# Kernel tuning notes

Hardware: AMD Instinct MI355X
Metric: run time of the kernel (lower is better)

Reference implementation:

```python
import jax, jax.numpy as jnp
import numpy as np

DIM = 1024
DIM_HEAD = 64
HEADS = 16
DIM_INNER = DIM_HEAD * HEADS  # 1024


def setup_inputs() -> dict:
    key = jax.random.key(0)
    k1, k2, k3 = jax.random.split(key, 3)
    b, n = 2, 2048
    x = jax.random.normal(k1, (b, n, DIM), dtype=jnp.float32)
    gamma = jnp.ones((DIM,), dtype=jnp.float32)
    # torch Linear weight [out,in] applied as x @ W.T; store pre-transposed [in,out]
    w_qkv = jax.random.normal(k2, (DIM, 3 * DIM_INNER), dtype=jnp.float32) * (DIM ** -0.5)
    w_out = jax.random.normal(k3, (DIM_INNER, DIM), dtype=jnp.float32) * (DIM_INNER ** -0.5)
    return {"x": x, "gamma": gamma, "w_qkv": w_qkv, "w_out": w_out}


def reference(x, gamma, w_qkv, w_out):
    h, d = HEADS, DIM_HEAD
    scale = d ** -0.5
    rms_scale = DIM ** 0.5
    # RMSNorm: F.normalize(x, dim=-1) * sqrt(dim) * gamma  (eps=1e-12 clamp on L2 norm)
    norm = jnp.maximum(jnp.linalg.norm(x, axis=-1, keepdims=True), 1e-12)
    xn = x / norm * rms_scale * gamma
    b, n, _ = x.shape
    qkv = xn @ w_qkv  # [b, n, 3*h*d]
    qkv = qkv.reshape(b, n, 3, h, d)
    q = qkv[:, :, 0].transpose(0, 2, 1, 3) * scale  # [b, h, n, d]
    k = qkv[:, :, 1].transpose(0, 2, 1, 3)
    v = qkv[:, :, 2].transpose(0, 2, 1, 3)
    sim = jnp.einsum('bhid,bhjd->bhij', q, k)  # [b, h, n, n]
    causal_mask = jnp.triu(jnp.ones((n, n), dtype=bool), k=1)
    neg = -jnp.finfo(sim.dtype).max
    sim = jnp.where(causal_mask, neg, sim)
    attn = jax.nn.softmax(sim, axis=-1)
    out = jnp.einsum('bhij,bhjd->bhid', attn, v)  # [b, h, n, d]
    out = out.transpose(0, 2, 1, 3).reshape(b, n, h * d)
    return out @ w_out
```

## Files before the change

kernel.cpp:

```cpp
#include <hip/hip_runtime.h>
#include <hip/hip_bf16.h>

typedef __bf16 bf16x8 __attribute__((ext_vector_type(8)));
typedef short s16x4 __attribute__((ext_vector_type(4)));
typedef float f32x4 __attribute__((ext_vector_type(4)));
typedef unsigned short u16x8 __attribute__((ext_vector_type(8)));

#define MFMA_K32(a, b, c) __builtin_amdgcn_mfma_f32_16x16x32_bf16(a, b, c, 0, 0, 0)

static __device__ __forceinline__ f32x4 mfma_k16(s16x4 a, s16x4 b, f32x4 c) {
#ifdef __HIP_DEVICE_COMPILE__
    return __builtin_amdgcn_mfma_f32_16x16x16bf16_1k(a, b, c, 0, 0, 0);
#else
    return c;
#endif
}

static __device__ __forceinline__ float fast_exp2(float x) {
#ifdef __HIP_DEVICE_COMPILE__
    return __builtin_amdgcn_exp2f(x);
#else
    return x;
#endif
}

static __device__ __forceinline__ void prio_hi() {
#ifdef __HIP_DEVICE_COMPILE__
    __builtin_amdgcn_s_setprio(1);
#endif
}
static __device__ __forceinline__ void prio_lo() {
#ifdef __HIP_DEVICE_COMPILE__
    __builtin_amdgcn_s_setprio(0);
#endif
}

#define GLL16(gp, lp)                                              \
    __builtin_amdgcn_global_load_lds(                              \
        (const __attribute__((address_space(1))) void*)(gp),       \
        (__attribute__((address_space(3))) void*)(lp), 16, 0, 0)

static __device__ __forceinline__ unsigned short f2bf(float f) {
    unsigned int u = __float_as_uint(f);
    u += 0x7fffu + ((u >> 16) & 1u);
    return (unsigned short)(u >> 16);
}

static __device__ __forceinline__ unsigned int cvtpk_bf16(float lo, float hi) {
#if defined(__HIP_DEVICE_COMPILE__) && __has_builtin(__builtin_amdgcn_cvt_pk_bf16_f32)
    typedef __bf16 bf16x2 __attribute__((ext_vector_type(2)));
    bf16x2 r = __builtin_amdgcn_cvt_pk_bf16_f32(lo, hi);
    return __builtin_bit_cast(unsigned int, r);
#else
    return (unsigned int)f2bf(lo) | ((unsigned int)f2bf(hi) << 16);
#endif
}

#define LOG2E 1.44269504088896340736f

__global__ __launch_bounds__(256) void prep_k(
    const float* __restrict__ x, const float* __restrict__ gamma,
    const float* __restrict__ w_qkv, const float* __restrict__ w_out,
    unsigned short* __restrict__ xn, unsigned short* __restrict__ wtq,
    unsigned short* __restrict__ wto) {
    __shared__ float sm[32][33];
    int bid = blockIdx.x, tid = threadIdx.x;
    if (bid < 4096) {
        const float* in;
        unsigned short* out;
        int R = 1024, C, bx, by;
        if (bid < 3072) { in = w_qkv; out = wtq; C = 3072; bx = bid % 96; by = bid / 96; }
        else { int b2 = bid - 3072; in = w_out; out = wto; C = 1024; bx = b2 % 32; by = b2 / 32; }
        int c0 = bx * 32, r0 = by * 32;
        int tr = tid >> 5, tc = tid & 31;
#pragma unroll
        for (int i = 0; i < 4; i++)
            sm[tr + i * 8][tc] = in[(size_t)(r0 + tr + i * 8) * C + c0 + tc];
        __syncthreads();
#pragma unroll
        for (int i = 0; i < 4; i++)
            out[(size_t)(c0 + tr + i * 8) * R + r0 + tc] = f2bf(sm[tc][tr + i * 8]);
    } else {
        int row = bid - 4096;
        const float* xr = x + (size_t)row * 1024;
        float4 v = *(const float4*)(xr + tid * 4);
        float ss = v.x * v.x + v.y * v.y + v.z * v.z + v.w * v.w;
#pragma unroll
        for (int off = 1; off < 64; off <<= 1) ss += __shfl_xor(ss, off, 64);
        if ((tid & 63) == 0) sm[0][tid >> 6] = ss;
        __syncthreads();
        float tot = sm[0][0] + sm[0][1] + sm[0][2] + sm[0][3];
        float f = 32.0f / fmaxf(sqrtf(tot), 1e-12f);
        float4 g = *(const float4*)(gamma + tid * 4);
        uint2 o;
        o.x = cvtpk_bf16(v.x * f * g.x, v.y * f * g.y);
        o.y = cvtpk_bf16(v.z * f * g.z, v.w * f * g.w);
        *(uint2*)(xn + (size_t)row * 1024 + tid * 4) = o;
    }
}

template <int MODE, int BM, int KS>
__global__ __launch_bounds__(256) void gemm_bt_k(
    const unsigned short* __restrict__ A, const unsigned short* __restrict__ BT,
    float* __restrict__ C, unsigned short* __restrict__ qw,
    unsigned short* __restrict__ kw, unsigned short* __restrict__ vw,
    int M, int N, int K) {
    constexpr int RT = 4;
    constexpr int CT = (BM == 128) ? 4 : 2;
    __shared__ unsigned short As[BM][32];
    __shared__ unsigned short Bs[128][32];
    int tid = threadIdx.x;
    int wave = tid >> 6, lane = tid & 63, quad = lane >> 4, l16 = lane & 15;
    int wrb, wcb;
    if constexpr (BM == 128) { wrb = (wave >> 1) * 64; wcb = (wave & 1) * 64; }
    else { wrb = 0; wcb = wave * 32; }
    int m0 = blockIdx.y * BM, n0 = blockIdx.x * 128;
    int k_beg = 0, k_end = K;
    if constexpr (KS > 1) {
        int kz = blockIdx.z;
        k_beg = kz * (K / KS);
        k_end = k_beg + K / KS;
    }
    int lrow = lane >> 2, lcol = (lane & 3) * 8;
    const unsigned short *Ag0, *Ag1 = nullptr;
    if constexpr (BM == 128) {
        Ag0 = A + (size_t)(m0 + wave * 32 + lrow) * K + lcol;
        Ag1 = A + (size_t)(m0 + wave * 32 + 16 + lrow) * K + lcol;
    } else {
        Ag0 = A + (size_t)(m0 + wave * 16 + lrow) * K + lcol;
    }
    const unsigned short* Bg0 = BT + (size_t)(n0 + wave * 32 + lrow) * K + lcol;
    const unsigned short* Bg1 = BT + (size_t)(n0 + wave * 32 + 16 + lrow) * K + lcol;
    f32x4 acc[RT][CT] = {};
    for (int k0 = k_beg; k0 < k_end; k0 += 32) {
        __syncthreads();
        if constexpr (BM == 128) {
            GLL16(Ag0 + k0, &As[wave * 32][0]);
            GLL16(Ag1 + k0, &As[wave * 32 + 16][0]);
        } else {
            GLL16(Ag0 + k0, &As[wave * 16][0]);
        }
        GLL16(Bg0 + k0, &Bs[wave * 32][0]);
        GLL16(Bg1 + k0, &Bs[wave * 32 + 16][0]);
        __syncthreads();
        bf16x8 af[RT], bfr[CT];
#pragma unroll
        for (int t = 0; t < RT; t++)
            af[t] = *(const bf16x8*)&As[wrb + t * 16 + l16][quad * 8];
#pragma unroll
        for (int t = 0; t < CT; t++)
            bfr[t] = *(const bf16x8*)&Bs[wcb + t * 16 + l16][quad * 8];
#pragma unroll
        for (int rt = 0; rt < RT; rt++)
#pragma unroll
            for (int ct = 0; ct < CT; ct++)
                acc[rt][ct] = MFMA_K32(af[rt], bfr[ct], acc[rt][ct]);
    }
#pragma unroll
    for (int rt = 0; rt < RT; rt++) {
        int mb = m0 + wrb + rt * 16 + quad * 4;
        int b = mb >> 11, nn = mb & 2047;
#pragma unroll
        for (int ct = 0; ct < CT; ct++) {
            int col = n0 + wcb + ct * 16 + l16;
            if (MODE == 0) {
                if constexpr (KS > 1) {
#pragma unroll
                    for (int r = 0; r < 4; r++)
                        atomicAdd(&C[(size_t)(mb + r) * N + col], acc[rt][ct][r]);
                } else {
#pragma unroll
                    for (int r = 0; r < 4; r++)
                        C[(size_t)(mb + r) * N + col] = acc[rt][ct][r];
                }
            } else {
                int sec = col >> 10, ci = col & 1023;
                int hh = ci >> 6, dd = ci & 63;
                int bh = b * 16 + hh;
                if (sec == 0) {
#pragma unroll
                    for (int r = 0; r < 4; r++)
                        qw[((size_t)bh * 2048 + nn + r) * 64 + dd] =
                            f2bf(acc[rt][ct][r] * (0.125f * LOG2E));
                } else if (sec == 1) {
#pragma unroll
                    for (int r = 0; r < 4; r++)
                        kw[((size_t)bh * 2048 + nn + r) * 64 + dd] = f2bf(acc[rt][ct][r]);
                } else {
                    uint2 pk;
                    pk.x = cvtpk_bf16(acc[rt][ct][0], acc[rt][ct][1]);
                    pk.y = cvtpk_bf16(acc[rt][ct][2], acc[rt][ct][3]);
                    *(uint2*)&vw[((size_t)bh * 64 + dd) * 2048 + nn] = pk;
                }
            }
        }
    }
}

__global__ __launch_bounds__(512, 4) void attn_k(
    const unsigned short* __restrict__ q, const unsigned short* __restrict__ k,
    const unsigned short* __restrict__ vt, unsigned short* __restrict__ o) {
    __shared__ __align__(16) char smem[38912];
    typedef unsigned short ush;
    ush(*Ks)[2][32][72] = (ush(*)[2][32][72])smem;
    ush(*Vt)[2][64][40] = (ush(*)[2][64][40])(smem + 18432);
    float(*Osm)[68] = (float(*)[68])smem;
    float* msm = (float*)(smem + 18432);
    float* lsm = msm + 64;

    int bh = blockIdx.x;
    int qt = 31 - (int)blockIdx.y;
    int tid = threadIdx.x, wave = tid >> 6, lane = tid & 63;
    int quad = lane >> 4, l16 = lane & 15;
    int g = wave >> 2, wq = wave & 3;
    int b = bh >> 4, h = bh & 15;
    const ush* qg = q + (size_t)bh * 2048 * 64;
    const ush* kg = k + (size_t)bh * 2048 * 64;
    const ush* vg = vt + (size_t)bh * 64 * 2048;

    int ti = wq * 64 + lane;
    int kr = ti >> 3, kc = (ti & 7) * 8;
    int vr = ti >> 2, vc = (ti & 3) * 8;
    const ush* Kg = kg + (size_t)kr * 64 + kc;
    const ush* Vg = vg + (size_t)vr * 2048 + vc;

    int row_l = wq * 16 + l16;
    int q0w = qt * 64 + wq * 16;
    bf16x8 bq[2];
#pragma unroll
    for (int ks = 0; ks < 2; ks++)
        bq[ks] = *(const bf16x8*)&qg[(size_t)(q0w + l16) * 64 + ks * 32 + quad * 8];

    f32x4 ot[4] = {};
    float mrun = -1e30f, lrun = 0.f;
    int nT = qt + 1;
    int kt0 = g ? (qt + 1) : 0;

    u16x8 pk, pv;
    pk = *(const u16x8*)(Kg + (size_t)kt0 * 2048);
    pv = *(const u16x8*)(Vg + kt0 * 32);
    *(u16x8*)&Ks[g][0][kr][kc] = pk;
    *(u16x8*)&Vt[g][0][vr][vc] = pv;
    __syncthreads();

    for (int i = 0; i < nT; i++) {
        int cb = i & 1, kt = kt0 + i;
        bool pf = (i + 1 < nT);
        if (pf) {
            pk = *(const u16x8*)(Kg + (size_t)(kt + 1) * 2048);
            pv = *(const u16x8*)(Vg + (kt + 1) * 32);
        }
        f32x4 sf[2];
        prio_hi();
#pragma unroll
        for (int ct = 0; ct < 2; ct++) {
            bf16x8 ak0 = *(const bf16x8*)&Ks[g][cb][ct * 16 + l16][quad * 8];
            bf16x8 ak1 = *(const bf16x8*)&Ks[g][cb][ct * 16 + l16][32 + quad * 8];
            f32x4 s = {};
            s = MFMA_K32(ak0, bq[0], s);
            s = MFMA_K32(ak1, bq[1], s);
            sf[ct] = s;
        }
        prio_lo();
        if (kt >= 2 * qt) {
#pragma unroll
            for (int ct = 0; ct < 2; ct++)
#pragma unroll
                for (int r = 0; r < 4; r++)
                    if (kt * 32 + ct * 16 + quad * 4 + r > qt * 64 + row_l)
                        sf[ct][r] = -1e30f;
        }
        float t0 = fmaxf(sf[0][0], sf[0][1]), t1 = fmaxf(sf[0][2], sf[0][3]);
        float t2 = fmaxf(sf[1][0], sf[1][1]), t3 = fmaxf(sf[1][2], sf[1][3]);
        float mx_l = fmaxf(fmaxf(t0, t1), fmaxf(t2, t3));
        if (__any(mx_l > mrun + 8.0f)) {
            float mx = fmaxf(mx_l, __shfl_xor(mx_l, 16, 64));
            mx = fmaxf(mx, __shfl_xor(mx, 32, 64));
            float mnew = fmaxf(mrun, mx);
            float al = fast_exp2(mrun - mnew);
            mrun = mnew;
            lrun *= al;
#pragma unroll
            for (int dt = 0; dt < 4; dt++)
#pragma unroll
                for (int r = 0; r < 4; r++) ot[dt][r] *= al;
        }
        float rs = 0.f;
#pragma unroll
        for (int ct = 0; ct < 2; ct++)
#pragma unroll
            for (int r = 0; r < 4; r++) {
                float p = fast_exp2(sf[ct][r] - mrun);
                sf[ct][r] = p;
                rs += p;
            }
        lrun += rs;
        s16x4 bpr[2];
#pragma unroll
        for (int ct = 0; ct < 2; ct++) {
            uint2 u;
            u.x = cvtpk_bf16(sf[ct][0], sf[ct][1]);
            u.y = cvtpk_bf16(sf[ct][2], sf[ct][3]);
            bpr[ct] = __builtin_bit_cast(s16x4, u);
        }
        prio_hi();
#pragma unroll
        for (int dt = 0; dt < 4; dt++) {
#pragma unroll
            for (int ct = 0; ct < 2; ct++) {
                s16x4 av = *(const s16x4*)&Vt[g][cb][dt * 16 + l16][ct * 16 + quad * 4];
                ot[dt] = mfma_k16(av, bpr[ct], ot[dt]);
            }
        }
        prio_lo();
        if (pf) {
            *(u16x8*)&Ks[g][1 - cb][kr][kc] = pk;
            *(u16x8*)&Vt[g][1 - cb][vr][vc] = pv;
        }
        __syncthreads();
    }

    lrun += __shfl_xor(lrun, 16, 64);
    lrun += __shfl_xor(lrun, 32, 64);

    if (g == 1) {
        msm[row_l] = mrun;
        lsm[row_l] = lrun;
#pragma unroll
        for (int dt = 0; dt < 4; dt++)
            *(f32x4*)&Osm[row_l][dt * 16 + quad * 4] = ot[dt];
    }
    __syncthreads();
    if (g == 0) {
        float m1 = msm[row_l], l1 = lsm[row_l];
        float mmax = fmaxf(mrun, m1);
        float a0 = fast_exp2(mrun - mmax), a1 = fast_exp2(m1 - mmax);
        float inv = 1.0f / (a0 * lrun + a1 * l1);
        float s0 = a0 * inv, s1 = a1 * inv;
        size_t rowbase = ((size_t)b * 2048 + qt * 64 + row_l) * 1024 + h * 64;
#pragma unroll
        for (int dt = 0; dt < 4; dt++) {
            f32x4 o1 = *(const f32x4*)&Osm[row_l][dt * 16 + quad * 4];
            uint2 pkk;
            pkk.x = cvtpk_bf16(ot[dt][0] * s0 + o1[0] * s1,
                               ot[dt][1] * s0 + o1[1] * s1);
            pkk.y = cvtpk_bf16(ot[dt][2] * s0 + o1[2] * s1,
                               ot[dt][3] * s0 + o1[3] * s1);
            *(uint2*)&o[rowbase + dt * 16 + quad * 4] = pkk;
        }
    }
}

extern "C" void kernel_launch(void* const* d_in, const int* in_sizes, int n_in,
                              void* d_out, int out_size, void* d_ws, size_t ws_size,
                              hipStream_t stream) {
    const float* x = (const float*)d_in[0];
    const float* gamma = (const float*)d_in[1];
    const float* w_qkv = (const float*)d_in[2];
    const float* w_out = (const float*)d_in[3];
    float* out = (float*)d_out;
    char* ws = (char*)d_ws;

    unsigned short* xn = (unsigned short*)(ws);
    unsigned short* wtq = (unsigned short*)(ws + 8388608);
    unsigned short* wto = (unsigned short*)(ws + 14680064);
    unsigned short* qw = (unsigned short*)(ws + 16777216);
    unsigned short* kw = (unsigned short*)(ws + 25165824);
    unsigned short* vw = (unsigned short*)(ws + 33554432);
    unsigned short* ao = xn;

    hipMemsetAsync(out, 0, (size_t)4096 * 1024 * 4, stream);

    prep_k<<<8192, 256, 0, stream>>>(x, gamma, w_qkv, w_out, xn, wtq, wto);
    gemm_bt_k<1, 128, 1><<<dim3(24, 32), 256, 0, stream>>>(xn, wtq, nullptr, qw, kw, vw,
                                                           4096, 3072, 1024);
    attn_k<<<dim3(32, 32), 512, 0, stream>>>(qw, kw, vw, ao);
    gemm_bt_k<0, 64, 2><<<dim3(8, 64, 2), 256, 0, stream>>>(ao, wto, out, nullptr,
                                                            nullptr, nullptr,
                                                            4096, 1024, 1024);
}
```

Baseline: 204.3 us.

## Use 64-key attention tiles with split-KV halves and drop split-K output GEMM

The attention kernel now processes 64-key tiles instead of 32, so each iteration does twice the MFMA work per barrier. The two wave groups split the key range into halves instead of one group idling past the diagonal, and masking runs only on the diagonal tile. The output projection GEMM no longer uses split-K with atomics, which removes the memset of the output buffer. Shared memory grows to about 72 KB per block, which may cut occupancy, and an idle group still waits at barriers when its half is shorter.

```diff
diff --git a/kernel.cpp b/kernel.cpp
--- a/kernel.cpp
+++ b/kernel.cpp
@@ -200,12 +200,12 @@
 __global__ __launch_bounds__(512, 4) void attn_k(
     const unsigned short* __restrict__ q, const unsigned short* __restrict__ k,
     const unsigned short* __restrict__ vt, unsigned short* __restrict__ o) {
-    __shared__ __align__(16) char smem[38912];
+    __shared__ __align__(16) char smem[73728];
     typedef unsigned short ush;
-    ush(*Ks)[2][32][72] = (ush(*)[2][32][72])smem;
-    ush(*Vt)[2][64][40] = (ush(*)[2][64][40])(smem + 18432);
+    ush(*Ks)[2][64][72] = (ush(*)[2][64][72])smem;
+    ush(*Vt)[2][64][72] = (ush(*)[2][64][72])(smem + 36864);
     float(*Osm)[68] = (float(*)[68])smem;
-    float* msm = (float*)(smem + 18432);
+    float* msm = (float*)(smem + 36864);
     float* lsm = msm + 64;
 
     int bh = blockIdx.x;
@@ -219,10 +219,9 @@
     const ush* vg = vt + (size_t)bh * 64 * 2048;
 
     int ti = wq * 64 + lane;
-    int kr = ti >> 3, kc = (ti & 7) * 8;
-    int vr = ti >> 2, vc = (ti & 3) * 8;
+    int kr = ti >> 2, kc = (ti & 3) * 8;
     const ush* Kg = kg + (size_t)kr * 64 + kc;
-    const ush* Vg = vg + (size_t)vr * 2048 + vc;
+    const ush* Vg = vg + (size_t)kr * 2048 + kc;
 
     int row_l = wq * 16 + l16;
     int q0w = qt * 64 + wq * 16;
@@ -233,89 +232,106 @@
 
     f32x4 ot[4] = {};
     float mrun = -1e30f, lrun = 0.f;
-    int nT = qt + 1;
-    int kt0 = g ? (qt + 1) : 0;
-
-    u16x8 pk, pv;
-    pk = *(const u16x8*)(Kg + (size_t)kt0 * 2048);
-    pv = *(const u16x8*)(Vg + kt0 * 32);
-    *(u16x8*)&Ks[g][0][kr][kc] = pk;
-    *(u16x8*)&Vt[g][0][vr][vc] = pv;
+    int nTot = qt + 1;
+    int nT0 = (nTot + 1) >> 1;
+    int myN = g ? (nTot - nT0) : nT0;
+    int kt0 = g ? nT0 : 0;
+    int L = nT0;
+
+    u16x8 pk0, pk1, pv0, pv1;
+    if (myN > 0) {
+        pk0 = *(const u16x8*)(Kg + (size_t)kt0 * 4096);
+        pk1 = *(const u16x8*)(Kg + (size_t)kt0 * 4096 + 32);
+        pv0 = *(const u16x8*)(Vg + kt0 * 64);
+        pv1 = *(const u16x8*)(Vg + kt0 * 64 + 32);
+        *(u16x8*)&Ks[g][0][kr][kc] = pk0;
+        *(u16x8*)&Ks[g][0][kr][kc + 32] = pk1;
+        *(u16x8*)&Vt[g][0][kr][kc] = pv0;
+        *(u16x8*)&Vt[g][0][kr][kc + 32] = pv1;
+    }
     __syncthreads();
 
-    for (int i = 0; i < nT; i++) {
+    for (int i = 0; i < L; i++) {
         int cb = i & 1, kt = kt0 + i;
-        bool pf = (i + 1 < nT);
+        bool act = (i < myN);
+        bool pf = (i + 1 < myN);
         if (pf) {
-            pk = *(const u16x8*)(Kg + (size_t)(kt + 1) * 2048);
-            pv = *(const u16x8*)(Vg + (kt + 1) * 32);
-        }
-        f32x4 sf[2];
-        prio_hi();
-#pragma unroll
-        for (int ct = 0; ct < 2; ct++) {
-            bf16x8 ak0 = *(const bf16x8*)&Ks[g][cb][ct * 16 + l16][quad * 8];
-            bf16x8 ak1 = *(const bf16x8*)&Ks[g][cb][ct * 16 + l16][32 + quad * 8];
-            f32x4 s = {};
-            s = MFMA_K32(ak0, bq[0], s);
-            s = MFMA_K32(ak1, bq[1], s);
-            sf[ct] = s;
-        }
-        prio_lo();
-        if (kt >= 2 * qt) {
-#pragma unroll
-            for (int ct = 0; ct < 2; ct++)
-#pragma unroll
-                for (int r = 0; r < 4; r++)
-                    if (kt * 32 + ct * 16 + quad * 4 + r > qt * 64 + row_l)
-                        sf[ct][r] = -1e30f;
-        }
-        float t0 = fmaxf(sf[0][0], sf[0][1]), t1 = fmaxf(sf[0][2], sf[0][3]);
-        float t2 = fmaxf(sf[1][0], sf[1][1]), t3 = fmaxf(sf[1][2], sf[1][3]);
-        float mx_l = fmaxf(fmaxf(t0, t1), fmaxf(t2, t3));
-        if (__any(mx_l > mrun + 8.0f)) {
-            float mx = fmaxf(mx_l, __shfl_xor(mx_l, 16, 64));
-            mx = fmaxf(mx, __shfl_xor(mx, 32, 64));
-            float mnew = fmaxf(mrun, mx);
-            float al = fast_exp2(mrun - mnew);
-            mrun = mnew;
-            lrun *= al;
-#pragma unroll
-            for (int dt = 0; dt < 4; dt++)
-#pragma unroll
-                for (int r = 0; r < 4; r++) ot[dt][r] *= al;
-        }
-        float rs = 0.f;
-#pragma unroll
-        for (int ct = 0; ct < 2; ct++)
-#pragma unroll
-            for (int r = 0; r < 4; r++) {
-                float p = fast_exp2(sf[ct][r] - mrun);
-                sf[ct][r] = p;
-                rs += p;
-            }
-        lrun += rs;
-        s16x4 bpr[2];
-#pragma unroll
-        for (int ct = 0; ct < 2; ct++) {
-            uint2 u;
-            u.x = cvtpk_bf16(sf[ct][0], sf[ct][1]);
-            u.y = cvtpk_bf16(sf[ct][2], sf[ct][3]);
-            bpr[ct] = __builtin_bit_cast(s16x4, u);
-        }
-        prio_hi();
-#pragma unroll
-        for (int dt = 0; dt < 4; dt++) {
-#pragma unroll
-            for (int ct = 0; ct < 2; ct++) {
-                s16x4 av = *(const s16x4*)&Vt[g][cb][dt * 16 + l16][ct * 16 + quad * 4];
-                ot[dt] = mfma_k16(av, bpr[ct], ot[dt]);
-            }
-        }
-        prio_lo();
+            pk0 = *(const u16x8*)(Kg + (size_t)(kt + 1) * 4096);
+            pk1 = *(const u16x8*)(Kg + (size_t)(kt + 1) * 4096 + 32);
+            pv0 = *(const u16x8*)(Vg + (kt + 1) * 64);
+            pv1 = *(const u16x8*)(Vg + (kt + 1) * 64 + 32);
+        }
+        if (act) {
+            f32x4 sf[4];
+            prio_hi();
+#pragma unroll
+            for (int ct = 0; ct < 4; ct++) {
+                bf16x8 ak0 = *(const bf16x8*)&Ks[g][cb][ct * 16 + l16][quad * 8];
+                bf16x8 ak1 = *(const bf16x8*)&Ks[g][cb][ct * 16 + l16][32 + quad * 8];
+                f32x4 s = {};
+                s = MFMA_K32(ak0, bq[0], s);
+                s = MFMA_K32(ak1, bq[1], s);
+                sf[ct] = s;
+            }
+            prio_lo();
+            if (kt == qt) {
+#pragma unroll
+                for (int ct = 0; ct < 4; ct++)
+#pragma unroll
+                    for (int r = 0; r < 4; r++)
+                        if (ct * 16 + quad * 4 + r > row_l) sf[ct][r] = -1e30f;
+            }
+            float m01 = fmaxf(fmaxf(fmaxf(sf[0][0], sf[0][1]), fmaxf(sf[0][2], sf[0][3])),
+                              fmaxf(fmaxf(sf[1][0], sf[1][1]), fmaxf(sf[1][2], sf[1][3])));
+            float m23 = fmaxf(fmaxf(fmaxf(sf[2][0], sf[2][1]), fmaxf(sf[2][2], sf[2][3])),
+                              fmaxf(fmaxf(sf[3][0], sf[3][1]), fmaxf(sf[3][2], sf[3][3])));
+            float mx_l = fmaxf(m01, m23);
+            if (__any(mx_l > mrun + 8.0f)) {
+                float mx = fmaxf(mx_l, __shfl_xor(mx_l, 16, 64));
+                mx = fmaxf(mx, __shfl_xor(mx, 32, 64));
+                float mnew = fmaxf(mrun, mx);
+                float al = fast_exp2(mrun - mnew);
+                mrun = mnew;
+                lrun *= al;
+#pragma unroll
+                for (int dt = 0; dt < 4; dt++)
+#pragma unroll
+                    for (int r = 0; r < 4; r++) ot[dt][r] *= al;
+            }
+            float rs = 0.f;
+#pragma unroll
+            for (int ct = 0; ct < 4; ct++)
+#pragma unroll
+                for (int r = 0; r < 4; r++) {
+                    float p = fast_exp2(sf[ct][r] - mrun);
+                    sf[ct][r] = p;
+                    rs += p;
+                }
+            lrun += rs;
+            s16x4 bpr[4];
+#pragma unroll
+            for (int ct = 0; ct < 4; ct++) {
+                uint2 u;
+                u.x = cvtpk_bf16(sf[ct][0], sf[ct][1]);
+                u.y = cvtpk_bf16(sf[ct][2], sf[ct][3]);
+                bpr[ct] = __builtin_bit_cast(s16x4, u);
+            }
+            prio_hi();
+#pragma unroll
+            for (int dt = 0; dt < 4; dt++) {
+#pragma unroll
+                for (int ct = 0; ct < 4; ct++) {
+                    s16x4 av = *(const s16x4*)&Vt[g][cb][dt * 16 + l16][ct * 16 + quad * 4];
+                    ot[dt] = mfma_k16(av, bpr[ct], ot[dt]);
+                }
+            }
+            prio_lo();
+        }
         if (pf) {
-            *(u16x8*)&Ks[g][1 - cb][kr][kc] = pk;
-            *(u16x8*)&Vt[g][1 - cb][vr][vc] = pv;
+            *(u16x8*)&Ks[g][1 - cb][kr][kc] = pk0;
+            *(u16x8*)&Ks[g][1 - cb][kr][kc + 32] = pk1;
+            *(u16x8*)&Vt[g][1 - cb][kr][kc] = pv0;
+            *(u16x8*)&Vt[g][1 - cb][kr][kc + 32] = pv1;
         }
         __syncthreads();
     }
@@ -369,13 +385,11 @@
     unsigned short* vw = (unsigned short*)(ws + 33554432);
     unsigned short* ao = xn;
 
-    hipMemsetAsync(out, 0, (size_t)4096 * 1024 * 4, stream);
-
     prep_k<<<8192, 256, 0, stream>>>(x, gamma, w_qkv, w_out, xn, wtq, wto);
     gemm_bt_k<1, 128, 1><<<dim3(24, 32), 256, 0, stream>>>(xn, wtq, nullptr, qw, kw, vw,
                                                            4096, 3072, 1024);
     attn_k<<<dim3(32, 32), 512, 0, stream>>>(qw, kw, vw, ao);
-    gemm_bt_k<0, 64, 2><<<dim3(8, 64, 2), 256, 0, stream>>>(ao, wto, out, nullptr,
-                                                            nullptr, nullptr,
-                                                            4096, 1024, 1024);
-}
+    gemm_bt_k<0, 64, 1><<<dim3(8, 64), 256, 0, stream>>>(ao, wto, out, nullptr,
+                                                         nullptr, nullptr,
+                                                         4096, 1024, 1024);
+}
```

After: 186.7 us. 1.09x faster.
